# Kernel tuning notes

Hardware: AMD Instinct MI355X
Metric: run time of the kernel (lower is better)

## Reference

```python
import jax, jax.numpy as jnp
import numpy as np

# Model dims (match init_kwargs)
HID = 1024   # hidden_size
H   = 16     # num_heads
DK  = 64     # head_dim (key)
DV  = 128    # head value dim = int(head_dim * expand_v)
VAL = H * DV # value_dim = 2048
CONV = 4     # short conv kernel size
EPS = 1e-6
NORM_EPS = 1e-5


def _causal_conv_silu(x, w):
    # x: [B,T,C], w: [C,K] depthwise causal conv, no bias, silu activation
    T = x.shape[1]
    K = w.shape[1]
    xp = jnp.pad(x, ((0, 0), (K - 1, 0), (0, 0)))
    y = sum(xp[:, i:i + T, :] * w[:, i] for i in range(K))
    return jax.nn.silu(y)


def setup_inputs() -> dict:
    key = jax.random.key(0)
    ks = jax.random.split(key, 16)
    s = 0.02
    rn = lambda k, sh: jax.random.normal(k, sh, jnp.float32)
    return {
        'hidden_states': rn(ks[0], (1, 2048, HID)),
        'norm_w': jnp.ones((HID,), jnp.float32),
        'q_w': rn(ks[1], (H * DK, HID)) * s,
        'k_w': rn(ks[2], (H * DK, HID)) * s,
        'v_w': rn(ks[3], (VAL, HID)) * s,
        'a_w': rn(ks[4], (H, HID)) * s,
        'b_w': rn(ks[5], (H, HID)) * s,
        'g_w': rn(ks[6], (VAL, HID)) * s,
        'dt_bias': jax.random.uniform(ks[7], (H,), jnp.float32, -2.0, 0.0),
        'A_log': jnp.log(jax.random.uniform(ks[8], (H,), jnp.float32, 1.0, 8.0)),
        'conv_q_w': rn(ks[9], (H * DK, CONV)) * 0.2,
        'conv_k_w': rn(ks[10], (H * DK, CONV)) * 0.2,
        'conv_v_w': rn(ks[11], (VAL, CONV)) * 0.2,
        'o_norm_w': jnp.ones((DV,), jnp.float32),
        'o_proj_w': rn(ks[12], (HID, VAL)) * s,
        'out_proj_w': rn(ks[13], (HID, HID)) * s,
    }


def reference(hidden_states, norm_w, q_w, k_w, v_w, a_w, b_w, g_w, dt_bias,
              A_log, conv_q_w, conv_k_w, conv_v_w, o_norm_w, o_proj_w, out_proj_w):
    B, T, D = hidden_states.shape
    # RMSNorm
    x = hidden_states * jax.lax.rsqrt(
        jnp.mean(hidden_states * hidden_states, -1, keepdims=True) + EPS) * norm_w

    # projections + causal depthwise short conv + silu
    q = _causal_conv_silu(x @ q_w.T, conv_q_w).reshape(B, T, H, DK)
    k = _causal_conv_silu(x @ k_w.T, conv_k_w).reshape(B, T, H, DK)
    v = _causal_conv_silu(x @ v_w.T, conv_v_w).reshape(B, T, H, DV)

    beta = jax.nn.sigmoid(x @ b_w.T)                       # [B,T,H]
    g = -jnp.exp(A_log) * jax.nn.softplus(x @ a_w.T + dt_bias)  # [B,T,H] log-decay

    # rank-1 DC removal on keys: (I - 1 1^T / DK) k, i.e. subtract per-head mean
    k = k - jnp.mean(k, -1, keepdims=True)

    # L2 normalize q, k along head dim; scale q
    q = q * jax.lax.rsqrt(jnp.sum(q * q, -1, keepdims=True) + EPS)
    k = k * jax.lax.rsqrt(jnp.sum(k * k, -1, keepdims=True) + EPS)
    q = q * (DK ** -0.5)

    # gated delta-rule recurrence over time (time-major scan)
    qT = q.transpose(1, 0, 2, 3)
    kT = k.transpose(1, 0, 2, 3)
    vT = v.transpose(1, 0, 2, 3)
    bT = beta.transpose(1, 0, 2)
    gT = g.transpose(1, 0, 2)

    def step(S, inp):
        qt, kt, vt, bt, gt = inp              # S: [B,H,DK,DV]
        S = S * jnp.exp(gt)[..., None, None]
        v_new = (vt - jnp.einsum('bhk,bhkv->bhv', kt, S)) * bt[..., None]
        S = S + jnp.einsum('bhk,bhv->bhkv', kt, v_new)
        o = jnp.einsum('bhk,bhkv->bhv', qt, S)
        return S, o

    S0 = jnp.zeros((B, H, DK, DV), x.dtype)
    _, oT = jax.lax.scan(step, S0, (qT, kT, vT, bT, gT))
    o = oT.transpose(1, 0, 2, 3)                           # [B,T,H,DV]

    # gated RMSNorm on output heads
    gate = (x @ g_w.T).reshape(B, T, H, DV)
    o = o * jax.lax.rsqrt(jnp.mean(o * o, -1, keepdims=True) + NORM_EPS) * o_norm_w
    o = o * jax.nn.silu(gate)

    o = o.reshape(B, T, VAL) @ o_proj_w.T                  # [B,T,HID]
    return o @ out_proj_w.T
```

## Files before the change

### kernel.cpp

```cpp
#include <hip/hip_runtime.h>
#include <math.h>

#define S72 72

typedef __bf16 bf16;
typedef __bf16 bf16x8 __attribute__((ext_vector_type(8)));
typedef __bf16 bf16x4v __attribute__((ext_vector_type(4)));
typedef __bf16 bf16x2v __attribute__((ext_vector_type(2)));
typedef float f32x4 __attribute__((ext_vector_type(4)));

__device__ __forceinline__ float wredsum(float v) {
#pragma unroll
  for (int off = 32; off > 0; off >>= 1) v += __shfl_xor(v, off, 64);
  return v;
}
__device__ __forceinline__ float sigmoidf_(float x) { return 1.f / (1.f + __expf(-x)); }

__device__ __forceinline__ int sxy(int row, int col) {
  return (row << 6) + ((((col >> 3) ^ (row & 7)) << 3) | (col & 7));
}
__device__ __forceinline__ int sx8(int row, int chunk) {
  return (row << 6) + ((chunk ^ (row & 7)) << 3);
}

__global__ __launch_bounds__(256) void k_pre(const float* __restrict__ h,
    const float* __restrict__ nw, const float* __restrict__ aw,
    const float* __restrict__ bw, const float* __restrict__ dtb,
    const float* __restrict__ alog, bf16* __restrict__ xb,
    float* __restrict__ graw, float* __restrict__ btb,
    const float* __restrict__ qw, const float* __restrict__ kw,
    const float* __restrict__ vw, const float* __restrict__ gw,
    const float* __restrict__ opw, const float* __restrict__ ow,
    bf16* qwb, bf16* kwb, bf16* vwb, bf16* gwb, bf16* opwb, bf16* owb) {
  __shared__ float red[4];
  __shared__ __align__(16) float xs[1024];
  int tid = threadIdx.x;
  if (blockIdx.x >= 2048) {
    long cb = blockIdx.x - 2048;
    for (long u = cb*256 + tid; u < 2359296; u += 4608l*256) {
      const float* src; bf16* dst; long l;
      if      (u <  262144) { src=qw;  dst=qwb;  l=u; }
      else if (u <  524288) { src=kw;  dst=kwb;  l=u-262144; }
      else if (u < 1048576) { src=vw;  dst=vwb;  l=u-524288; }
      else if (u < 1572864) { src=gw;  dst=gwb;  l=u-1048576; }
      else if (u < 2097152) { src=opw; dst=opwb; l=u-1572864; }
      else                  { src=ow;  dst=owb;  l=u-2097152; }
      float4 s = *(const float4*)(src + l*4);
      bf16x4v b; b[0]=(bf16)s.x; b[1]=(bf16)s.y; b[2]=(bf16)s.z; b[3]=(bf16)s.w;
      *(bf16x4v*)(dst + l*4) = b;
    }
    return;
  }
  int t = blockIdx.x;
  float4 hv = *(const float4*)(h + (size_t)t*1024 + tid*4);
  float ss = hv.x*hv.x + hv.y*hv.y + hv.z*hv.z + hv.w*hv.w;
  float wsum = wredsum(ss);
  if ((tid & 63) == 0) red[tid >> 6] = wsum;
  __syncthreads();
  float tot = red[0] + red[1] + red[2] + red[3];
  float rs = rsqrtf(tot * (1.f/1024.f) + 1e-6f);
  float4 w4 = *(const float4*)(nw + tid*4);
  float4 y;
  y.x = hv.x*rs*w4.x; y.y = hv.y*rs*w4.y; y.z = hv.z*rs*w4.z; y.w = hv.w*rs*w4.w;
  *(float4*)(xs + tid*4) = y;
  bf16x4v b; b[0]=(bf16)y.x; b[1]=(bf16)y.y; b[2]=(bf16)y.z; b[3]=(bf16)y.w;
  *(bf16x4v*)(xb + (size_t)t*1024 + tid*4) = b;
  __syncthreads();
  int wave = tid >> 6, lane = tid & 63;
  const float4* x4 = (const float4*)xs;
#pragma unroll
  for (int hi = 0; hi < 4; ++hi) {
    int hh = wave*4 + hi;
    float sa = 0.f, sb = 0.f;
#pragma unroll
    for (int i = 0; i < 4; ++i) {
      float4 xv = x4[i*64 + lane];
      float4 av = *(const float4*)(aw + hh*1024 + i*256 + lane*4);
      float4 bv = *(const float4*)(bw + hh*1024 + i*256 + lane*4);
      sa += xv.x*av.x + xv.y*av.y + xv.z*av.z + xv.w*av.w;
      sb += xv.x*bv.x + xv.y*bv.y + xv.z*bv.z + xv.w*bv.w;
    }
    sa = wredsum(sa); sb = wredsum(sb);
    if (lane == 0) {
      float ap = sa + dtb[hh];
      float sp = (ap > 20.f) ? ap : log1pf(expf(ap));
      graw[t*16 + hh] = -expf(alog[hh]) * sp;
      btb[t*16 + hh] = 1.f / (1.f + expf(-sb));
    }
  }
}

template <typename OutT>
__device__ __forceinline__ void gemm_body(const bf16* __restrict__ A,
    const bf16* __restrict__ B, OutT* __restrict__ C, int N, int K, int m0, int n0) {
  __shared__ bf16 As[2][128*32];
  __shared__ bf16 Bs[2][128*32];
  const int tid = threadIdx.x, lane = tid & 63, wave = tid >> 6;
  const int wm = (wave >> 1) * 64, wn = (wave & 1) * 64;
  const int srow = wave*16 + (lane >> 2);
  const int swl = (((lane & 3) ^ ((lane >> 3) & 3))) * 8;
  const int sdst = (lane & 3) * 8;
  const int quad = lane >> 4, l16 = lane & 15;
  const int sw = (l16 >> 1) & 3;
  f32x4 acc[4][4] = {};
  const int nk = K >> 5;
#pragma unroll
  for (int i = 0; i < 2; ++i) {
    int r = i*64 + srow;
    __builtin_amdgcn_global_load_lds(
      (__attribute__((address_space(1))) void*)(A + (size_t)(m0 + r)*K + swl),
      (__attribute__((address_space(3))) void*)(&As[0][r*32 + sdst]), 16, 0, 0);
    __builtin_amdgcn_global_load_lds(
      (__attribute__((address_space(1))) void*)(B + (size_t)(n0 + r)*K + swl),
      (__attribute__((address_space(3))) void*)(&Bs[0][r*32 + sdst]), 16, 0, 0);
  }
  for (int kt = 0; kt < nk; ++kt) {
    const int cur = kt & 1;
    __syncthreads();
    bf16x8 af[4], bfr[4];
#pragma unroll
    for (int mt = 0; mt < 4; ++mt)
      af[mt] = *(const bf16x8*)(&As[cur][(wm + mt*16 + l16)*32 + (quad ^ sw)*8]);
#pragma unroll
    for (int nt = 0; nt < 4; ++nt)
      bfr[nt] = *(const bf16x8*)(&Bs[cur][(wn + nt*16 + l16)*32 + (quad ^ sw)*8]);
    if (kt + 1 < nk) {
      int k0 = (kt + 1) << 5;
#pragma unroll
      for (int i = 0; i < 2; ++i) {
        int r = i*64 + srow;
        __builtin_amdgcn_global_load_lds(
          (__attribute__((address_space(1))) void*)(A + (size_t)(m0 + r)*K + k0 + swl),
          (__attribute__((address_space(3))) void*)(&As[cur^1][r*32 + sdst]), 16, 0, 0);
        __builtin_amdgcn_global_load_lds(
          (__attribute__((address_space(1))) void*)(B + (size_t)(n0 + r)*K + k0 + swl),
          (__attribute__((address_space(3))) void*)(&Bs[cur^1][r*32 + sdst]), 16, 0, 0);
      }
    }
#pragma unroll
    for (int mt = 0; mt < 4; ++mt)
#pragma unroll
      for (int nt = 0; nt < 4; ++nt)
        acc[mt][nt] = __builtin_amdgcn_mfma_f32_16x16x32_bf16(af[mt], bfr[nt], acc[mt][nt], 0, 0, 0);
  }
#pragma unroll
  for (int mt = 0; mt < 4; ++mt)
#pragma unroll
    for (int nt = 0; nt < 4; ++nt)
#pragma unroll
      for (int r = 0; r < 4; ++r) {
        int row = m0 + wm + mt*16 + quad*4 + r;
        int col = n0 + wn + nt*16 + l16;
        C[(size_t)row*N + col] = (OutT)acc[mt][nt][r];
      }
}

__global__ __launch_bounds__(256) void k_gemm_proj(const bf16* __restrict__ A,
    const bf16* __restrict__ qwb, const bf16* __restrict__ kwb,
    const bf16* __restrict__ vwb, const bf16* __restrict__ gwb,
    bf16* __restrict__ qpre, bf16* __restrict__ kpre,
    bf16* __restrict__ vpre, bf16* __restrict__ gpre) {
  int bx = blockIdx.x;
  const bf16* B; bf16* C; int N, xt;
  if      (bx <  8) { B = qwb; C = qpre; N = 1024; xt = bx; }
  else if (bx < 16) { B = kwb; C = kpre; N = 1024; xt = bx - 8; }
  else if (bx < 32) { B = vwb; C = vpre; N = 2048; xt = bx - 16; }
  else              { B = gwb; C = gpre; N = 2048; xt = bx - 32; }
  gemm_body<bf16>(A, B, C, N, 1024, blockIdx.y*128, xt*128);
}

template <typename OutT>
__global__ __launch_bounds__(256) void k_gemm_bt64(const bf16* __restrict__ A,
    const bf16* __restrict__ B, OutT* __restrict__ C, int N, int K) {
  __shared__ bf16 As[2][128*32];
  __shared__ bf16 Bs[2][64*32];
  const int tid = threadIdx.x, lane = tid & 63, wave = tid >> 6;
  const int wm = wave * 32;
  const int srow = wave*16 + (lane >> 2);
  const int swl = (((lane & 3) ^ ((lane >> 3) & 3))) * 8;
  const int sdst = (lane & 3) * 8;
  const int quad = lane >> 4, l16 = lane & 15;
  const int sw = (l16 >> 1) & 3;
  const int m0 = blockIdx.y * 128, n0 = blockIdx.x * 64;
  f32x4 acc[2][4] = {};
  const int nk = K >> 5;
#pragma unroll
  for (int i = 0; i < 2; ++i) {
    int r = i*64 + srow;
    __builtin_amdgcn_global_load_lds(
      (__attribute__((address_space(1))) void*)(A + (size_t)(m0 + r)*K + swl),
      (__attribute__((address_space(3))) void*)(&As[0][r*32 + sdst]), 16, 0, 0);
  }
  __builtin_amdgcn_global_load_lds(
    (__attribute__((address_space(1))) void*)(B + (size_t)(n0 + srow)*K + swl),
    (__attribute__((address_space(3))) void*)(&Bs[0][srow*32 + sdst]), 16, 0, 0);
  for (int kt = 0; kt < nk; ++kt) {
    const int cur = kt & 1;
    __syncthreads();
    bf16x8 af[2], bfr[4];
#pragma unroll
    for (int mt = 0; mt < 2; ++mt)
      af[mt] = *(const bf16x8*)(&As[cur][(wm + mt*16 + l16)*32 + (quad ^ sw)*8]);
#pragma unroll
    for (int nt = 0; nt < 4; ++nt)
      bfr[nt] = *(const bf16x8*)(&Bs[cur][(nt*16 + l16)*32 + (quad ^ sw)*8]);
    if (kt + 1 < nk) {
      int k0 = (kt + 1) << 5;
#pragma unroll
      for (int i = 0; i < 2; ++i) {
        int r = i*64 + srow;
        __builtin_amdgcn_global_load_lds(
          (__attribute__((address_space(1))) void*)(A + (size_t)(m0 + r)*K + k0 + swl),
          (__attribute__((address_space(3))) void*)(&As[cur^1][r*32 + sdst]), 16, 0, 0);
      }
      __builtin_amdgcn_global_load_lds(
        (__attribute__((address_space(1))) void*)(B + (size_t)(n0 + srow)*K + k0 + swl),
        (__attribute__((address_space(3))) void*)(&Bs[cur^1][srow*32 + sdst]), 16, 0, 0);
    }
#pragma unroll
    for (int mt = 0; mt < 2; ++mt)
#pragma unroll
      for (int nt = 0; nt < 4; ++nt)
        acc[mt][nt] = __builtin_amdgcn_mfma_f32_16x16x32_bf16(af[mt], bfr[nt], acc[mt][nt], 0, 0, 0);
  }
#pragma unroll
  for (int mt = 0; mt < 2; ++mt)
#pragma unroll
    for (int nt = 0; nt < 4; ++nt)
#pragma unroll
      for (int r = 0; r < 4; ++r) {
        int row = m0 + wm + mt*16 + quad*4 + r;
        int col = n0 + nt*16 + l16;
        C[(size_t)row*N + col] = (OutT)acc[mt][nt][r];
      }
}

template<int NT>
__device__ __forceinline__ void mm_band(const bf16* A_lds, const bf16* B_lds,
    int w16, int cb, int l16, int quad, f32x4* acc) {
#pragma unroll
  for (int n = 0; n < NT; ++n) { acc[n][0]=0.f; acc[n][1]=0.f; acc[n][2]=0.f; acc[n][3]=0.f; }
#pragma unroll
  for (int kt = 0; kt < 2; ++kt) {
    bf16x8 af = *(const bf16x8*)(A_lds + sx8(w16 + l16, kt*4 + quad));
#pragma unroll
    for (int n = 0; n < NT; ++n) {
      bf16x8 bf = *(const bf16x8*)(B_lds + sx8(cb + n*16 + l16, kt*4 + quad));
      acc[n] = __builtin_amdgcn_mfma_f32_16x16x32_bf16(af, bf, acc[n], 0, 0, 0);
    }
  }
}

__global__ __launch_bounds__(512) void k_prepass(
    const bf16* __restrict__ qpre, const bf16* __restrict__ kpre,
    const bf16* __restrict__ vpre, const float* __restrict__ cqw,
    const float* __restrict__ ckw, const float* __restrict__ cvw,
    const float* __restrict__ graw, const float* __restrict__ beta,
    bf16* __restrict__ EF, float* __restrict__ dSl, float* __restrict__ obuf) {
  const int bx = blockIdx.x, c = bx >> 4, h = bx & 15, tid = threadIdx.x;
  const int t0 = c * 64;
  const int wave = tid >> 6, lane = tid & 63, l16 = lane & 15, quad = lane >> 4;
  const int w16 = (wave >> 1) * 16;
  const int chh = wave & 1;
  const int r0 = wave * 8;

  __shared__ bf16 SM[36864];
  __shared__ float bs[64], bts_s[64], es[64], gms[64];
  bf16* Kr    = SM;
  bf16* powR0 = SM + 4096;
  bf16* prod0 = SM + 8192;
  bf16* T2T   = SM + 12288;
  bf16* powT0 = SM + 16384;
  bf16* powR1 = SM + 20480;
  bf16* powT1 = SM + 24576;
  bf16* prod1 = SM + 28672;
  bf16* qbf   = SM + 32768;
  bf16* VT   = SM;
  bf16* VlT  = SM + 8192;
  bf16* KT   = powT0;
  bf16* KbT  = powR1;
  bf16* Pm   = powT1;
  bf16* WR   = prod0;
  bf16* Mrow = prod1;

  if (tid < 64) {
    float g = graw[(size_t)(t0 + tid)*16 + h];
    float b = g;
#pragma unroll
    for (int off = 1; off < 64; off <<= 1) {
      float p = __shfl_up(b, off, 64);
      if (tid >= off) b += p;
    }
    bs[tid] = b;
    bts_s[tid] = beta[(size_t)(t0 + tid)*16 + h];
    float b63 = __shfl(b, 63, 64);
    es[tid] = __expf(b63 - b);
    gms[tid] = __expf(b);
  }

  float kreg[8], vreg[16];
  {
    float4 wq  = *(const float4*)(cqw + (h*64 + lane)*4);
    float4 wk  = *(const float4*)(ckw + (h*64 + lane)*4);
    float tv[11];
#pragma unroll
    for (int j = 0; j < 11; ++j) {
      int tg = t0 + r0 + j - 3;
      tv[j] = (tg >= 0) ? (float)qpre[(size_t)tg*1024 + h*64 + lane] : 0.f;
    }
#pragma unroll
    for (int rr = 0; rr < 8; ++rr) {
      float y = tv[rr]*wq.x + tv[rr+1]*wq.y + tv[rr+2]*wq.z + tv[rr+3]*wq.w;
      y = y * sigmoidf_(y);
      float ssq = wredsum(y*y);
      y *= rsqrtf(ssq + 1e-6f) * 0.125f;
      qbf[sxy(r0+rr, lane)] = (bf16)y;
    }
#pragma unroll
    for (int j = 0; j < 11; ++j) {
      int tg = t0 + r0 + j - 3;
      tv[j] = (tg >= 0) ? (float)kpre[(size_t)tg*1024 + h*64 + lane] : 0.f;
    }
#pragma unroll
    for (int rr = 0; rr < 8; ++rr) {
      float y = tv[rr]*wk.x + tv[rr+1]*wk.y + tv[rr+2]*wk.z + tv[rr+3]*wk.w;
      y = y * sigmoidf_(y);
      float m = wredsum(y) * (1.f/64.f);
      y -= m;
      float ssq = wredsum(y*y);
      y *= rsqrtf(ssq + 1e-6f);
      kreg[rr] = y;
      Kr[sxy(r0+rr, lane)] = (bf16)y;
    }
#pragma unroll
    for (int hf = 0; hf < 2; ++hf) {
      float4 wv = *(const float4*)(cvw + (h*128 + hf*64 + lane)*4);
#pragma unroll
      for (int j = 0; j < 11; ++j) {
        int tg = t0 + r0 + j - 3;
        tv[j] = (tg >= 0) ? (float)vpre[(size_t)tg*2048 + h*128 + hf*64 + lane] : 0.f;
      }
#pragma unroll
      for (int rr = 0; rr < 8; ++rr) {
        float y = tv[rr]*wv.x + tv[rr+1]*wv.y + tv[rr+2]*wv.z + tv[rr+3]*wv.w;
        vreg[hf*8+rr] = y * sigmoidf_(y);
      }
    }
  }
  __syncthreads();

  {
    f32x4 acc[2];
    mm_band<2>(Kr, Kr, w16, chh*32, l16, quad, acc);
#pragma unroll
    for (int n = 0; n < 2; ++n) {
      int col = chh*32 + n*16 + l16;
      bf16x4v tv;
#pragma unroll
      for (int r = 0; r < 4; ++r) {
        int row = w16 + quad*4 + r;
        float nv = 0.f;
        if (row > col) nv = -bts_s[row] * __expf(bs[row] - bs[col]) * acc[n][r];
        bf16 nb = (bf16)nv;
        powR0[sxy(row, col)] = nb;
        tv[r] = nb;
        prod0[sxy(row, col)] = (row == col) ? (bf16)1.f : nb;
      }
      *(bf16x4v*)(powT0 + sxy(col, w16 + quad*4)) = tv;
    }
  }
  __syncthreads();

  int pc = 0, rc = 0;
#pragma unroll 1
  for (int i = 1; i <= 5; ++i) {
    bf16* sqA = pc ? powR1 : powR0;
    bf16* sqB = pc ? powT1 : powT0;
    bf16* sqRo = pc ? powR0 : powR1;
    bf16* sqTo = pc ? powT0 : powT1;
    {
      f32x4 acc[2];
      mm_band<2>(sqA, sqB, w16, chh*32, l16, quad, acc);
#pragma unroll
      for (int n = 0; n < 2; ++n) {
        int col = chh*32 + n*16 + l16;
        bf16x4v tv;
#pragma unroll
        for (int r = 0; r < 4; ++r) {
          int row = w16 + quad*4 + r;
          bf16 vb = (bf16)acc[n][r];
          sqRo[sxy(row, col)] = vb;
          tv[r] = vb;
        }
        *(bf16x4v*)(sqTo + sxy(col, w16 + quad*4)) = tv;
      }
    }
    __syncthreads();
    bf16* prA = rc ? prod1 : prod0;
    bf16* prO = rc ? prod0 : prod1;
    {
      f32x4 acc[2];
      mm_band<2>(prA, sqTo, w16, chh*32, l16, quad, acc);
#pragma unroll
      for (int n = 0; n < 2; ++n) {
        int col = chh*32 + n*16 + l16;
        bf16x4v tv;
#pragma unroll
        for (int r = 0; r < 4; ++r) {
          int row = w16 + quad*4 + r;
          float val = acc[n][r] + (float)prA[sxy(row, col)];
          prO[sxy(row, col)] = (bf16)val;
          tv[r] = (bf16)(val * bts_s[col] * gms[col]);
        }
        if (i == 5) *(bf16x4v*)(T2T + sxy(col, w16 + quad*4)) = tv;
      }
    }
    __syncthreads();
    pc ^= 1; rc ^= 1;
  }

#pragma unroll
  for (int rr = 0; rr < 8; ++rr) {
    KT[sxy(lane, r0+rr)]  = (bf16)kreg[rr];
    KbT[sxy(lane, r0+rr)] = (bf16)(kreg[rr] * es[r0+rr]);
  }
  {
    f32x4 acc[2];
#pragma unroll
    for (int n = 0; n < 2; ++n) { acc[n][0]=0.f; acc[n][1]=0.f; acc[n][2]=0.f; acc[n][3]=0.f; }
#pragma unroll
    for (int kt = 0; kt < 2; ++kt) {
      bf16x8 af = *(const bf16x8*)(qbf + sx8(w16 + l16, kt*4 + quad));
#pragma unroll
      for (int n = 0; n < 2; ++n) {
        bf16x8 bf = *(const bf16x8*)(Kr + sx8(chh*32 + n*16 + l16, kt*4 + quad));
        acc[n] = __builtin_amdgcn_mfma_f32_16x16x32_bf16(af, bf, acc[n], 0, 0, 0);
      }
    }
#pragma unroll
    for (int n = 0; n < 2; ++n) {
      int col = chh*32 + n*16 + l16;
#pragma unroll
      for (int r = 0; r < 4; ++r) {
        int row = w16 + quad*4 + r;
        float pv = (row >= col) ? __expf(bs[row] - bs[col]) * acc[n][r] : 0.f;
        Pm[sxy(row, col)] = (bf16)pv;
      }
    }
  }
  __syncthreads();

  {
    f32x4 acc[2];
    mm_band<2>(KbT, T2T, w16, chh*32, l16, quad, acc);
#pragma unroll
    for (int n = 0; n < 2; ++n) {
      int col = chh*32 + n*16 + l16;
#pragma unroll
      for (int r = 0; r < 4; ++r)
        WR[sxy(w16 + quad*4 + r, col)] = (bf16)acc[n][r];
    }
  }
#pragma unroll
  for (int hf = 0; hf < 2; ++hf)
#pragma unroll
    for (int rr = 0; rr < 8; ++rr)
      VT[sxy(hf*64 + lane, r0+rr)] = (bf16)(bts_s[r0+rr] * vreg[hf*8+rr]);
  __syncthreads();
  {
    f32x4 acc[2];
    mm_band<2>(WR, KT, w16, chh*32, l16, quad, acc);
    float gC = gms[63];
    size_t eb = (size_t)bx * 13824;
#pragma unroll
    for (int n = 0; n < 2; ++n) {
      int col = chh*32 + n*16 + l16;
#pragma unroll
      for (int r = 0; r < 4; ++r) {
        int row = w16 + quad*4 + r;
        float ev = ((row == col) ? gC : 0.f) - acc[n][r];
        bf16 eh = (bf16)ev;
        EF[eb + row*S72 + col] = eh;
        EF[eb + 4608 + row*S72 + col] = (bf16)(ev - (float)eh);
      }
    }
  }
  __syncthreads();
  {
    f32x4 acc[2];
    mm_band<2>(Pm, T2T, w16, chh*32, l16, quad, acc);
#pragma unroll
    for (int n = 0; n < 2; ++n) {
      int col = chh*32 + n*16 + l16;
#pragma unroll
      for (int r = 0; r < 4; ++r)
        WR[sxy(w16 + quad*4 + r, col)] = (bf16)acc[n][r];
    }
  }
  __syncthreads();
  {
    f32x4 acc[2];
    mm_band<2>(WR, KT, w16, chh*32, l16, quad, acc);
    size_t eb = (size_t)bx * 13824;
#pragma unroll
    for (int n = 0; n < 2; ++n) {
      int col = chh*32 + n*16 + l16;
#pragma unroll
      for (int r = 0; r < 4; ++r) {
        int row = w16 + quad*4 + r;
        float qv = (float)qbf[sxy(row, col)];
        EF[eb + 9216 + row*S72 + col] = (bf16)(gms[row]*qv - acc[n][r]);
      }
    }
  }
  __syncthreads();
  {
    f32x4 acc[4];
    mm_band<4>(Mrow, VT, w16, chh*64, l16, quad, acc);
#pragma unroll
    for (int n = 0; n < 4; ++n) {
      int col = chh*64 + n*16 + l16;
      bf16x4v tv;
#pragma unroll
      for (int r = 0; r < 4; ++r) tv[r] = (bf16)acc[n][r];
      *(bf16x4v*)(VlT + sxy(col, w16 + quad*4)) = tv;
    }
  }
  __syncthreads();
  {
    f32x4 acc[4];
    mm_band<4>(KbT, VlT, w16, chh*64, l16, quad, acc);
#pragma unroll
    for (int n = 0; n < 4; ++n) {
      int col = chh*64 + n*16 + l16;
#pragma unroll
      for (int r = 0; r < 4; ++r)
        dSl[(size_t)bx*8192 + (size_t)(w16 + quad*4 + r)*128 + col] = acc[n][r];
    }
  }
  {
    f32x4 acc[4];
    mm_band<4>(Pm, VlT, w16, chh*64, l16, quad, acc);
#pragma unroll
    for (int n = 0; n < 4; ++n) {
      int col = chh*64 + n*16 + l16;
#pragma unroll
      for (int r = 0; r < 4; ++r)
        obuf[(size_t)(t0 + w16 + quad*4 + r)*2048 + h*128 + col] = acc[n][r];
    }
  }
}

__global__ __launch_bounds__(256) void k_seq(const bf16* __restrict__ EF,
    const float* __restrict__ dSl, float* __restrict__ osb) {
  const int h = blockIdx.x >> 2, dq = blockIdx.x & 3;
  const int tid = threadIdx.x, wave = tid >> 6, lane = tid & 63;
  const int l16 = lane & 15, quad = lane >> 4;
  const int mb = wave * 16;
  __shared__ bf16 ebuf[2][13824];
  __shared__ bf16 Sthi[32*S72], Stlo[32*S72];
  for (int i = tid; i < 2304; i += 256) { Sthi[i] = (bf16)0.f; Stlo[i] = (bf16)0.f; }
  {
    const bf16* efg = EF + (size_t)h * 13824;
    for (int i = tid; i < 1728; i += 256)
      __builtin_amdgcn_global_load_lds(
        (__attribute__((address_space(1))) void*)(efg + i*8),
        (__attribute__((address_space(3))) void*)(&ebuf[0][i*8]), 16, 0, 0);
  }
  float dsv[8];
  {
    size_t base = (size_t)h*8192 + dq*32;
#pragma unroll
    for (int nt = 0; nt < 2; ++nt)
#pragma unroll
      for (int r = 0; r < 4; ++r)
        dsv[nt*4+r] = dSl[base + (size_t)(mb + quad*4 + r)*128 + nt*16 + l16];
  }
  __syncthreads();
#pragma unroll 1
  for (int c = 0; c < 32; ++c) {
    const int cur = c & 1, nxt = cur ^ 1;
    float dsn[8] = {};
    if (c + 1 < 32) {
      const bf16* efg = EF + (size_t)((c+1)*16 + h) * 13824;
      for (int i = tid; i < 1728; i += 256)
        __builtin_amdgcn_global_load_lds(
          (__attribute__((address_space(1))) void*)(efg + i*8),
          (__attribute__((address_space(3))) void*)(&ebuf[nxt][i*8]), 16, 0, 0);
      size_t base = (size_t)((c+1)*16 + h)*8192 + dq*32;
#pragma unroll
      for (int nt = 0; nt < 2; ++nt)
#pragma unroll
        for (int r = 0; r < 4; ++r)
          dsn[nt*4+r] = dSl[base + (size_t)(mb + quad*4 + r)*128 + nt*16 + l16];
    }
    const bf16* Eh = &ebuf[cur][0];
    const bf16* El = &ebuf[cur][4608];
    const bf16* Ff = &ebuf[cur][9216];
    bf16x8 bh[2][2], bl[2][2];
#pragma unroll
    for (int nt = 0; nt < 2; ++nt)
#pragma unroll
      for (int kt = 0; kt < 2; ++kt) {
        bh[nt][kt] = *(const bf16x8*)(Sthi + (nt*16 + l16)*S72 + kt*32 + quad*8);
        bl[nt][kt] = *(const bf16x8*)(Stlo + (nt*16 + l16)*S72 + kt*32 + quad*8);
      }
    f32x4 accS[2], accO[2];
#pragma unroll
    for (int nt = 0; nt < 2; ++nt) {
#pragma unroll
      for (int r = 0; r < 4; ++r) accS[nt][r] = dsv[nt*4+r];
      accO[nt][0]=0.f; accO[nt][1]=0.f; accO[nt][2]=0.f; accO[nt][3]=0.f;
    }
#pragma unroll
    for (int kt = 0; kt < 2; ++kt) {
      bf16x8 aeh = *(const bf16x8*)(Eh + (mb + l16)*S72 + kt*32 + quad*8);
      bf16x8 ael = *(const bf16x8*)(El + (mb + l16)*S72 + kt*32 + quad*8);
      bf16x8 aff = *(const bf16x8*)(Ff + (mb + l16)*S72 + kt*32 + quad*8);
#pragma unroll
      for (int nt = 0; nt < 2; ++nt) {
        accS[nt] = __builtin_amdgcn_mfma_f32_16x16x32_bf16(aeh, bh[nt][kt], accS[nt], 0, 0, 0);
        accS[nt] = __builtin_amdgcn_mfma_f32_16x16x32_bf16(aeh, bl[nt][kt], accS[nt], 0, 0, 0);
        accS[nt] = __builtin_amdgcn_mfma_f32_16x16x32_bf16(ael, bh[nt][kt], accS[nt], 0, 0, 0);
        accO[nt] = __builtin_amdgcn_mfma_f32_16x16x32_bf16(aff, bh[nt][kt], accO[nt], 0, 0, 0);
        accO[nt] = __builtin_amdgcn_mfma_f32_16x16x32_bf16(aff, bl[nt][kt], accO[nt], 0, 0, 0);
      }
    }
    __syncthreads();
    {
      int t0 = c*64;
#pragma unroll
      for (int nt = 0; nt < 2; ++nt)
#pragma unroll
        for (int r = 0; r < 4; ++r)
          osb[(size_t)(t0 + mb + quad*4 + r)*2048 + h*128 + dq*32 + nt*16 + l16] = accO[nt][r];
    }
#pragma unroll
    for (int nt = 0; nt < 2; ++nt) {
      bf16x4v hv, lv;
#pragma unroll
      for (int r = 0; r < 4; ++r) {
        float v = accS[nt][r];
        bf16 hb = (bf16)v;
        hv[r] = hb;
        lv[r] = (bf16)(v - (float)hb);
      }
      *(bf16x4v*)(Sthi + (nt*16 + l16)*S72 + mb + quad*4) = hv;
      *(bf16x4v*)(Stlo + (nt*16 + l16)*S72 + mb + quad*4) = lv;
    }
#pragma unroll
    for (int i = 0; i < 8; ++i) dsv[i] = dsn[i];
    __syncthreads();
  }
}

__global__ __launch_bounds__(64) void k_gatenorm(const float* __restrict__ o,
    const float* __restrict__ os, const bf16* __restrict__ gpre,
    const float* __restrict__ onw, bf16* __restrict__ og) {
  int t = blockIdx.x, hh = blockIdx.y, lane = threadIdx.x;
  size_t base = (size_t)t*2048 + hh*128 + lane*2;
  float2 o2 = *(const float2*)(o + base);
  float2 s2 = *(const float2*)(os + base);
  o2.x += s2.x; o2.y += s2.y;
  float ss = wredsum(o2.x*o2.x + o2.y*o2.y);
  float rs = rsqrtf(ss * (1.f/128.f) + 1e-5f);
  float2 nw = *(const float2*)(onw + lane*2);
  bf16x2v g2 = *(const bf16x2v*)(gpre + base);
  float g0 = (float)g2[0], g1 = (float)g2[1];
  float r0 = o2.x * rs * nw.x * (g0 * sigmoidf_(g0));
  float r1 = o2.y * rs * nw.y * (g1 * sigmoidf_(g1));
  bf16x2v b; b[0] = (bf16)r0; b[1] = (bf16)r1;
  *(bf16x2v*)(og + base) = b;
}

extern "C" void kernel_launch(void* const* d_in, const int* in_sizes, int n_in,
                              void* d_out, int out_size, void* d_ws, size_t ws_size,
                              hipStream_t stream) {
  const float* hs   = (const float*)d_in[0];
  const float* nw   = (const float*)d_in[1];
  const float* qw   = (const float*)d_in[2];
  const float* kw   = (const float*)d_in[3];
  const float* vw   = (const float*)d_in[4];
  const float* aw   = (const float*)d_in[5];
  const float* bw   = (const float*)d_in[6];
  const float* gw   = (const float*)d_in[7];
  const float* dtb  = (const float*)d_in[8];
  const float* alog = (const float*)d_in[9];
  const float* cqw  = (const float*)d_in[10];
  const float* ckw  = (const float*)d_in[11];
  const float* cvw  = (const float*)d_in[12];
  const float* onw  = (const float*)d_in[13];
  const float* opw  = (const float*)d_in[14];
  const float* ow   = (const float*)d_in[15];
  float* out = (float*)d_out;

  char* p = (char*)d_ws;
  auto alloc = [&](size_t bytes) { char* r = p; p += (bytes + 255) & ~255ull; return r; };
  bf16*  xb    = (bf16*) alloc((size_t)2048*1024*2);
  bf16*  qwb   = (bf16*) alloc((size_t)1024*1024*2);
  bf16*  kwb   = (bf16*) alloc((size_t)1024*1024*2);
  bf16*  vwb   = (bf16*) alloc((size_t)2048*1024*2);
  bf16*  gwb   = (bf16*) alloc((size_t)2048*1024*2);
  bf16*  opwb  = (bf16*) alloc((size_t)1024*2048*2);
  bf16*  owb   = (bf16*) alloc((size_t)1024*1024*2);
  bf16*  qpre  = (bf16*) alloc((size_t)2048*1024*2);
  bf16*  kpre  = (bf16*) alloc((size_t)2048*1024*2);
  bf16*  vpre  = (bf16*) alloc((size_t)2048*2048*2);
  bf16*  gpre  = (bf16*) alloc((size_t)2048*2048*2);
  float* graw  = (float*)alloc((size_t)2048*16*4);
  float* btb   = (float*)alloc((size_t)2048*16*4);
  float* ob    = (float*)alloc((size_t)2048*2048*4);
  bf16*  ogb   = (bf16*) alloc((size_t)2048*2048*2);
  bf16*  h1b   = (bf16*) alloc((size_t)2048*1024*2);
  bf16*  EF    = (bf16*) alloc((size_t)512*13824*2);
  float* osb   = (float*)alloc((size_t)512*8192*4);
  float* dSl   = (float*)xb;

  k_pre<<<2048+4608, 256, 0, stream>>>(hs, nw, aw, bw, dtb, alog, xb, graw, btb,
                                       qw, kw, vw, gw, opw, ow,
                                       qwb, kwb, vwb, gwb, opwb, owb);
  k_gemm_proj<<<dim3(48,16,1), 256, 0, stream>>>(xb, qwb, kwb, vwb, gwb, qpre, kpre, vpre, gpre);
  k_prepass<<<512, 512, 0, stream>>>(qpre, kpre, vpre, cqw, ckw, cvw, graw, btb, EF, dSl, ob);
  k_seq<<<64, 256, 0, stream>>>(EF, dSl, osb);
  k_gatenorm<<<dim3(2048,16,1), 64, 0, stream>>>(ob, osb, gpre, onw, ogb);
  k_gemm_bt64<bf16><<<dim3(16,16,1), 256, 0, stream>>>(ogb, opwb, h1b, 1024, 2048);
  k_gemm_bt64<float><<<dim3(16,16,1), 256, 0, stream>>>(h1b, owb, out, 1024, 1024);
}
```

Measured before the change: 283.9 us.

## Load k_seq chunk operands straight into registers and remap block-to-head order

Measured after the change: 272.0 us. 4.2% less time.

```diff
diff --git a/kernel.cpp b/kernel.cpp
--- a/kernel.cpp
+++ b/kernel.cpp
@@ -553,50 +553,44 @@
 
 __global__ __launch_bounds__(256) void k_seq(const bf16* __restrict__ EF,
     const float* __restrict__ dSl, float* __restrict__ osb) {
-  const int h = blockIdx.x >> 2, dq = blockIdx.x & 3;
+  const int bid = blockIdx.x;
+  const int h = (bid & 7) + 8*((bid >> 3) & 1);
+  const int dq = bid >> 4;
   const int tid = threadIdx.x, wave = tid >> 6, lane = tid & 63;
   const int l16 = lane & 15, quad = lane >> 4;
   const int mb = wave * 16;
-  __shared__ bf16 ebuf[2][13824];
   __shared__ bf16 Sthi[32*S72], Stlo[32*S72];
   for (int i = tid; i < 2304; i += 256) { Sthi[i] = (bf16)0.f; Stlo[i] = (bf16)0.f; }
-  {
-    const bf16* efg = EF + (size_t)h * 13824;
-    for (int i = tid; i < 1728; i += 256)
-      __builtin_amdgcn_global_load_lds(
-        (__attribute__((address_space(1))) void*)(efg + i*8),
-        (__attribute__((address_space(3))) void*)(&ebuf[0][i*8]), 16, 0, 0);
-  }
-  float dsv[8];
-  {
-    size_t base = (size_t)h*8192 + dq*32;
+
+  const size_t arow = (size_t)(mb + l16)*S72 + quad*8;
+  const size_t drow = (size_t)dq*32 + (size_t)(mb + quad*4)*128 + l16;
+
+  bf16x8 eh[2][2], el[2][2], ff[2][2];
+  float dsv[2][8];
+
+  auto loadEF = [&](int c, int sl) {
+    const bf16* base = EF + (size_t)(c*16 + h)*13824 + arow;
+#pragma unroll
+    for (int kt = 0; kt < 2; ++kt) {
+      eh[sl][kt] = *(const bf16x8*)(base + kt*32);
+      el[sl][kt] = *(const bf16x8*)(base + 4608 + kt*32);
+      ff[sl][kt] = *(const bf16x8*)(base + 9216 + kt*32);
+    }
+    const float* db = dSl + (size_t)(c*16 + h)*8192 + drow;
 #pragma unroll
     for (int nt = 0; nt < 2; ++nt)
 #pragma unroll
       for (int r = 0; r < 4; ++r)
-        dsv[nt*4+r] = dSl[base + (size_t)(mb + quad*4 + r)*128 + nt*16 + l16];
-  }
-  __syncthreads();
-#pragma unroll 1
+        dsv[sl][nt*4+r] = db[(size_t)r*128 + nt*16];
+  };
+
+  loadEF(0, 0);
+  asm volatile("s_waitcnt lgkmcnt(0)" ::: "memory");
+  __builtin_amdgcn_s_barrier();
+
+#pragma unroll 2
   for (int c = 0; c < 32; ++c) {
     const int cur = c & 1, nxt = cur ^ 1;
-    float dsn[8] = {};
-    if (c + 1 < 32) {
-      const bf16* efg = EF + (size_t)((c+1)*16 + h) * 13824;
-      for (int i = tid; i < 1728; i += 256)
-        __builtin_amdgcn_global_load_lds(
-          (__attribute__((address_space(1))) void*)(efg + i*8),
-          (__attribute__((address_space(3))) void*)(&ebuf[nxt][i*8]), 16, 0, 0);
-      size_t base = (size_t)((c+1)*16 + h)*8192 + dq*32;
-#pragma unroll
-      for (int nt = 0; nt < 2; ++nt)
-#pragma unroll
-        for (int r = 0; r < 4; ++r)
-          dsn[nt*4+r] = dSl[base + (size_t)(mb + quad*4 + r)*128 + nt*16 + l16];
-    }
-    const bf16* Eh = &ebuf[cur][0];
-    const bf16* El = &ebuf[cur][4608];
-    const bf16* Ff = &ebuf[cur][9216];
     bf16x8 bh[2][2], bl[2][2];
 #pragma unroll
     for (int nt = 0; nt < 2; ++nt)
@@ -605,28 +599,28 @@
         bh[nt][kt] = *(const bf16x8*)(Sthi + (nt*16 + l16)*S72 + kt*32 + quad*8);
         bl[nt][kt] = *(const bf16x8*)(Stlo + (nt*16 + l16)*S72 + kt*32 + quad*8);
       }
+    if (c + 1 < 32) loadEF(c + 1, nxt);
+
     f32x4 accS[2], accO[2];
 #pragma unroll
     for (int nt = 0; nt < 2; ++nt) {
 #pragma unroll
-      for (int r = 0; r < 4; ++r) accS[nt][r] = dsv[nt*4+r];
+      for (int r = 0; r < 4; ++r) accS[nt][r] = dsv[cur][nt*4+r];
       accO[nt][0]=0.f; accO[nt][1]=0.f; accO[nt][2]=0.f; accO[nt][3]=0.f;
     }
 #pragma unroll
     for (int kt = 0; kt < 2; ++kt) {
-      bf16x8 aeh = *(const bf16x8*)(Eh + (mb + l16)*S72 + kt*32 + quad*8);
-      bf16x8 ael = *(const bf16x8*)(El + (mb + l16)*S72 + kt*32 + quad*8);
-      bf16x8 aff = *(const bf16x8*)(Ff + (mb + l16)*S72 + kt*32 + quad*8);
 #pragma unroll
       for (int nt = 0; nt < 2; ++nt) {
-        accS[nt] = __builtin_amdgcn_mfma_f32_16x16x32_bf16(aeh, bh[nt][kt], accS[nt], 0, 0, 0);
-        accS[nt] = __builtin_amdgcn_mfma_f32_16x16x32_bf16(aeh, bl[nt][kt], accS[nt], 0, 0, 0);
-        accS[nt] = __builtin_amdgcn_mfma_f32_16x16x32_bf16(ael, bh[nt][kt], accS[nt], 0, 0, 0);
-        accO[nt] = __builtin_amdgcn_mfma_f32_16x16x32_bf16(aff, bh[nt][kt], accO[nt], 0, 0, 0);
-        accO[nt] = __builtin_amdgcn_mfma_f32_16x16x32_bf16(aff, bl[nt][kt], accO[nt], 0, 0, 0);
-      }
-    }
-    __syncthreads();
+        accS[nt] = __builtin_amdgcn_mfma_f32_16x16x32_bf16(eh[cur][kt], bh[nt][kt], accS[nt], 0, 0, 0);
+        accS[nt] = __builtin_amdgcn_mfma_f32_16x16x32_bf16(eh[cur][kt], bl[nt][kt], accS[nt], 0, 0, 0);
+        accS[nt] = __builtin_amdgcn_mfma_f32_16x16x32_bf16(el[cur][kt], bh[nt][kt], accS[nt], 0, 0, 0);
+        accO[nt] = __builtin_amdgcn_mfma_f32_16x16x32_bf16(ff[cur][kt], bh[nt][kt], accO[nt], 0, 0, 0);
+        accO[nt] = __builtin_amdgcn_mfma_f32_16x16x32_bf16(ff[cur][kt], bl[nt][kt], accO[nt], 0, 0, 0);
+      }
+    }
+    asm volatile("s_waitcnt lgkmcnt(0)" ::: "memory");
+    __builtin_amdgcn_s_barrier();
     {
       int t0 = c*64;
 #pragma unroll
@@ -648,9 +642,8 @@
       *(bf16x4v*)(Sthi + (nt*16 + l16)*S72 + mb + quad*4) = hv;
       *(bf16x4v*)(Stlo + (nt*16 + l16)*S72 + mb + quad*4) = lv;
     }
-#pragma unroll
-    for (int i = 0; i < 8; ++i) dsv[i] = dsn[i];
-    __syncthreads();
+    asm volatile("s_waitcnt lgkmcnt(0)" ::: "memory");
+    __builtin_amdgcn_s_barrier();
   }
 }
 
```
